# Kernel optimization log

Measured on AMD Instinct MI355X. Metric: run time of the kernel, lower is better.

## Reference

```python
import jax, jax.numpy as jnp
import numpy as np

STU, ITEM, CONC, D = 50000, 20000, 2000, 128
E_CC, E_IC, E_SI = 40000, 80000, 1000000


def _gat(tgt_x, src_x, e_src, e_dst, n_tgt, W, att_l, att_r, slope=0.2):
    # single-head GATConv, aggr='add', concat with heads=1 -> [n_tgt, D]
    if W is not None:
        xl = src_x @ W.T  # lin_l applied to source
        xr = tgt_x @ W.T  # lin_l shared for target (in_channels is int)
        # noqa: torch module uses lin_l for both when in_channels is int
    else:
        xl, xr = src_x, tgt_x
    sl = xl @ att_l  # [n_src]
    sr = xr @ att_r  # [n_tgt]
    e = sl[e_src] + sr[e_dst]
    e = jnp.where(e > 0, e, slope * e)  # leaky_relu
    # segment softmax over edges grouped by target node
    m = jax.ops.segment_max(e, e_dst, num_segments=n_tgt)
    m = jnp.where(jnp.isfinite(m), m, 0.0)
    ex = jnp.exp(e - m[e_dst])
    den = jax.ops.segment_sum(ex, e_dst, num_segments=n_tgt) + 1e-16
    alpha = ex / den[e_dst]
    return jax.ops.segment_sum(xl[e_src] * alpha[:, None], e_dst, num_segments=n_tgt)


def setup_inputs():
    key = jax.random.key(0)
    ks = jax.random.split(key, 40)
    s = 1.0 / np.sqrt(D)
    n = lambda k, sh, sc=1.0: jax.random.normal(k, sh, jnp.float32) * sc
    return {
        'stu_x': n(ks[0], (STU, D)),
        'item_x': n(ks[1], (ITEM, D)),
        'conc_x': n(ks[2], (CONC, D)),
        'stu_raw_x': n(ks[3], (STU, D)),
        'W_cc': n(ks[4], (D, D), s), 'al_cc': n(ks[5], (D,), s), 'ar_cc': n(ks[6], (D,), s),
        'W_ic': n(ks[7], (D, D), s), 'al_ic': n(ks[8], (D,), s), 'ar_ic': n(ks[9], (D,), s),
        'al_cce': n(ks[10], (D,), s), 'ar_cce': n(ks[11], (D,), s),
        'al_ice': n(ks[12], (D,), s), 'ar_ice': n(ks[13], (D,), s),
        'W_ci': n(ks[14], (D, D), s), 'al_ci': n(ks[15], (D,), s), 'ar_ci': n(ks[16], (D,), s),
        'W_si': n(ks[17], (D, D), s), 'al_si': n(ks[18], (D,), s), 'ar_si': n(ks[19], (D,), s),
        'w_ci_att': n(ks[20], (2 * D,), s), 'w_si_att': n(ks[21], (2 * D,), s),
        'W_is': n(ks[22], (D, D), s), 'al_is': n(ks[23], (D,), s), 'ar_is': n(ks[24], (D,), s),
        'cc_src': jax.random.randint(ks[25], (E_CC,), 0, CONC),
        'cc_dst': jax.random.randint(ks[26], (E_CC,), 0, CONC),
        'ic_item': jax.random.randint(ks[27], (E_IC,), 0, ITEM),
        'ic_conc': jax.random.randint(ks[28], (E_IC,), 0, CONC),
        'si_stu': jax.random.randint(ks[29], (E_SI,), 0, STU),
        'si_item': jax.random.randint(ks[30], (E_SI,), 0, ITEM),
    }


def reference(stu_x, item_x, conc_x, stu_raw_x,
              W_cc, al_cc, ar_cc, W_ic, al_ic, ar_ic,
              al_cce, ar_cce, al_ice, ar_ice,
              W_ci, al_ci, ar_ci, W_si, al_si, ar_si,
              w_ci_att, w_si_att, W_is, al_is, ar_is,
              cc_src, cc_dst, ic_item, ic_conc, si_stu, si_item):
    # --- concept fusion ---
    c1 = _gat(conc_x, conc_x, cc_src, cc_dst, CONC, W_cc, al_cc, ar_cc)   # inter_conc_conc
    c2 = _gat(conc_x, item_x, ic_item, ic_conc, CONC, W_ic, al_ic, ar_ic) # inter_item_conc
    e1 = _gat(conc_x, c1, cc_src, cc_dst, CONC, None, al_cce, ar_cce)     # exter_conc_conc (no lin)
    e2 = _gat(conc_x, c2, cc_src, cc_dst, CONC, None, al_ice, ar_ice)     # exter_item_conc (no lin)
    conc_fused = conc_x + e1 + e2
    # --- item fusion ---
    i1 = _gat(item_x, conc_x, ic_conc, ic_item, ITEM, W_ci, al_ci, ar_ci) # inter_conc_item
    i2 = _gat(item_x, stu_x, si_stu, si_item, ITEM, W_si, al_si, ar_si)   # inter_stu_item
    # softmax over dim=1 of an [N,1] tensor (as in the torch code): equals 1.0
    att1 = jax.nn.softmax((jnp.concatenate([i1, item_x], axis=1) @ w_ci_att)[:, None], axis=1)
    att2 = jax.nn.softmax((jnp.concatenate([i2, item_x], axis=1) @ w_si_att)[:, None], axis=1)
    item_fused = item_x + att1 * i1 + att2 * i2
    # --- student fusion (uses raw data['stu'].x as target) ---
    s1 = _gat(stu_raw_x, item_x, si_item, si_stu, STU, W_is, al_is, ar_is)
    stu_fused = stu_raw_x + s1
    return (conc_fused, item_fused, stu_fused)
```

## Files before the change

### kernel.cpp

```cpp
#include <hip/hip_runtime.h>

#define CONC_N 2000
#define ITEM_N 20000
#define STU_N  50000
#define NE_CC  40000
#define NE_IC  80000
#define NE_SI  1000000
#define TBUCK  382

typedef unsigned int uint;
typedef unsigned short ushort;
typedef __attribute__((ext_vector_type(8))) short bf16x8;
typedef __attribute__((ext_vector_type(4))) float f32x4;

__device__ __forceinline__ ushort f2bf(float f) {
  uint u = __float_as_uint(f);
  uint r = (u + 0x7FFFu + ((u >> 16) & 1u)) >> 16;
  return (ushort)r;
}

__device__ __forceinline__ bf16x8 packfrag(float4 lo, float4 hi) {
  union { bf16x8 s; uint u[4]; } p;
  p.u[0] = (uint)f2bf(lo.x) | ((uint)f2bf(lo.y) << 16);
  p.u[1] = (uint)f2bf(lo.z) | ((uint)f2bf(lo.w) << 16);
  p.u[2] = (uint)f2bf(hi.x) | ((uint)f2bf(hi.y) << 16);
  p.u[3] = (uint)f2bf(hi.z) | ((uint)f2bf(hi.w) << 16);
  return p.s;
}


struct CsrG {
  const int* dst; const int* src;
  unsigned* keys; int* srcs; int* offs;
  int E, n, shift, nbuck, tb, sb;
};
struct CsrGs { CsrG g[5]; };


struct ProjDesc { const float* W; const float* a; float* out; };
struct SetupArgs {
  ProjDesc p[10];
  CsrGs G;
  int* pcnt;
  const float* wsrc[5];
  ushort* wdst[5];
};

__global__ __launch_bounds__(256) void setup_k(SetupArgs A) {
  int b = blockIdx.x;
  int tid = threadIdx.x;
  if (b < 10) {
    __shared__ float Wl[128 * 132];
    __shared__ float a_s[128];
    ProjDesc d = A.p[b];
    #pragma unroll
    for (int i = 0; i < 16; ++i) {
      int s = tid + i * 256;
      int row = s >> 5, c4 = s & 31;
      float4 w = *(const float4*)&d.W[s * 4];
      float* dst = &Wl[row * 132 + c4 * 4];
      dst[0] = w.x; dst[1] = w.y; dst[2] = w.z; dst[3] = w.w;
    }
    if (tid < 128) a_s[tid] = d.a[tid];
    __syncthreads();
    if (tid < 128) {
      float acc = 0.f;
      #pragma unroll 4
      for (int j = 0; j < 128; ++j) acc += Wl[j * 132 + tid] * a_s[j];
      d.out[tid] = acc;
    }
    return;
  }
  if (b >= 170) {
    int wi = b - 170;
    const float* Ws = A.wsrc[wi];
    ushort* Wd = A.wdst[wi];
    for (int rec = tid; rec < 2048; rec += 256) {
      int lane = rec & 63;
      int kk = (rec >> 6) & 3;
      int nt = rec >> 8;
      int x = lane & 15, g = lane >> 4;
      const float* src = &Ws[(nt * 16 + x) * 128 + kk * 32 + 4 * g];
      float4 lo = *(const float4*)src;
      float4 hi = *(const float4*)(src + 16);
      bf16x8 pk = packfrag(lo, hi);
      *(bf16x8*)&Wd[rec * 8] = pk;
    }
    return;
  }
  int bsel = b - 10;
  int gi = bsel >> 5, blk = bsel & 31;
  CsrG g = A.G.g[gi];
  __shared__ int lcnt[128];
  if (tid < 128) lcnt[tid] = 0;
  __syncthreads();
  int chunk = (g.E + 31) >> 5;
  int e0 = blk * chunk, e1 = min(g.E, e0 + chunk);
  for (int e = e0 + tid; e < e1; e += 256)
    atomicAdd(&lcnt[g.dst[e] >> g.shift], 1);
  __syncthreads();
  if (tid < 128) A.pcnt[bsel * 128 + tid] = lcnt[tid];
}


__global__ __launch_bounds__(512) void csr_scan(CsrGs G, const int* __restrict__ pcnt,
                                                int* __restrict__ cur, int* __restrict__ bases) {
  __shared__ int lc[TBUCK];
  __shared__ int lb[TBUCK + 5];
  int tid = threadIdx.x, lane = tid & 63, wv = tid >> 6;
  if (tid < TBUCK) {
    int gi = 0;
    #pragma unroll
    for (int k = 1; k < 5; ++k) if (tid >= G.g[k].tb) gi = k;
    int b = tid - G.g[gi].tb;
    int s = 0;
    for (int blk = 0; blk < 32; ++blk) s += pcnt[((gi << 5) + blk) * 128 + b];
    lc[tid] = s;
  }
  __syncthreads();
  if (wv < 5) {
    CsrG g = G.g[wv];
    int carry = 0;
    for (int base = 0; base < g.nbuck; base += 64) {
      int idx = base + lane;
      int v = (idx < g.nbuck) ? lc[g.tb + idx] : 0;
      int incl = v;
      #pragma unroll
      for (int o = 1; o < 64; o <<= 1) {
        int y = __shfl_up(incl, o);
        if (lane >= o) incl += y;
      }
      if (idx < g.nbuck) lb[g.sb + idx] = carry + incl - v;
      carry += __shfl(incl, 63);
    }
    if (lane == 0) lb[g.sb + g.nbuck] = carry;
  }
  __syncthreads();
  if (tid < TBUCK + 5) bases[tid] = lb[tid];
  if (tid < TBUCK) {
    int gi = 0;
    for (int k = 1; k < 5; ++k) if (tid >= G.g[k].tb) gi = k;
    cur[tid] = lb[tid + gi];
  }
  if (tid < 5) G.g[tid].offs[G.g[tid].n] = G.g[tid].E;
}


struct GemmDesc { const float* X; ushort* Y; int n, b0; const float* dv[6]; float* dq[6]; };
struct BigC {
  GemmDesc g[5];
  int gemm_blocks;
  const float* rx; const float* rv; float* ro; int rnb;
};

__device__ void partition_body(const CsrGs& G, int* __restrict__ cur, int gi, int bx,
                               int nbx, unsigned char* smem) {
  CsrG g = G.g[gi];
  unsigned* ck = (unsigned*)smem;
  unsigned char* cb = smem + 16384;
  int* lcnt = (int*)(smem + 20480);
  int* lcur = (int*)(smem + 20992);
  int tid = threadIdx.x;
  unsigned dmask = (1u << g.shift) - 1;
  for (int c0 = bx * 4096; c0 < g.E; c0 += nbx * 4096) {
    if (tid < 128) lcnt[tid] = 0;
    __syncthreads();
    #pragma unroll
    for (int i = 0; i < 16; ++i) {
      int e = c0 + i * 256 + tid;
      if (e < g.E) {
        int d = g.dst[e], s = g.src[e];
        int b = d >> g.shift;
        ck[i * 256 + tid] = ((unsigned)(d & dmask) << 16) | (unsigned)s;
        cb[i * 256 + tid] = (unsigned char)b;
        atomicAdd(&lcnt[b], 1);
      } else cb[i * 256 + tid] = 255;
    }
    __syncthreads();
    if (tid < g.nbuck && lcnt[tid] > 0) lcur[tid] = atomicAdd(&cur[g.tb + tid], lcnt[tid]);
    __syncthreads();
    #pragma unroll
    for (int i = 0; i < 16; ++i) {
      int b = cb[i * 256 + tid];
      if (b != 255) {
        int pos = atomicAdd(&lcur[b], 1);
        g.keys[pos] = ck[i * 256 + tid];
      }
    }
    __syncthreads();
  }
}

template <int NV>
__device__ void gemm_bodyT(const GemmDesc& gd, const ushort* __restrict__ Wf, int blk) {
  int tid = threadIdx.x;
  int lane = tid & 63, wv = tid >> 6;
  int x = lane & 15, g = lane >> 4;
  int row = blk * 64 + wv * 16 + x;
  const float* xr = &gd.X[(size_t)(row < gd.n ? row : 0) * 128];
  bf16x8 afrag[4];
  float dacc[NV == 0 ? 1 : NV];
  #pragma unroll
  for (int v = 0; v < NV; ++v) dacc[v] = 0.f;
  #pragma unroll
  for (int kk = 0; kk < 4; ++kk) {
    float4 lo = *(const float4*)&xr[kk * 32 + 4 * g];
    float4 hi = *(const float4*)&xr[kk * 32 + 16 + 4 * g];
    afrag[kk] = packfrag(lo, hi);
    #pragma unroll
    for (int v = 0; v < NV; ++v) {
      const float* vp = gd.dv[v];
      float4 vlo = *(const float4*)&vp[kk * 32 + 4 * g];
      float4 vhi = *(const float4*)&vp[kk * 32 + 16 + 4 * g];
      dacc[v] += lo.x * vlo.x + lo.y * vlo.y + lo.z * vlo.z + lo.w * vlo.w
               + hi.x * vhi.x + hi.y * vhi.y + hi.z * vhi.z + hi.w * vhi.w;
    }
  }
  #pragma unroll
  for (int v = 0; v < NV; ++v) {
    float dsum = dacc[v];
    dsum += __shfl_xor(dsum, 16);
    dsum += __shfl_xor(dsum, 32);
    if (lane < 16 && row < gd.n) gd.dq[v][row] = dsum;
  }
  f32x4 acc[8];
  #pragma unroll
  for (int t = 0; t < 8; ++t) acc[t] = (f32x4){0.f, 0.f, 0.f, 0.f};
  #pragma unroll
  for (int nt = 0; nt < 8; ++nt) {
    #pragma unroll
    for (int kk = 0; kk < 4; ++kk) {
      union { uint4 u; bf16x8 s; } bu;
      bu.u = *(const uint4*)&Wf[(size_t)((nt * 4 + kk) * 64 + lane) * 8];
      acc[nt] = __builtin_amdgcn_mfma_f32_16x16x32_bf16(afrag[kk], bu.s, acc[nt], 0, 0, 0);
    }
  }
  int orow = blk * 64 + wv * 16 + 4 * g;
  #pragma unroll
  for (int r = 0; r < 4; ++r) {
    int gr = orow + r;
    if (gr < gd.n) {
      #pragma unroll
      for (int nt = 0; nt < 8; ++nt)
        gd.Y[(size_t)gr * 128 + nt * 16 + x] = f2bf(acc[nt][r]);
    }
  }
}

__device__ void rdot_body(const float* __restrict__ x, const float* __restrict__ v,
                          float* __restrict__ o, int n, int blk, int nblk) {
  int lane = threadIdx.x & 63;
  int wid = (blk * 256 + threadIdx.x) >> 6;
  int nw = nblk * 4;
  float va = v[lane], vb = v[64 + lane];
  for (int r = wid; r < n; r += nw) {
    float a = x[r * 128 + lane] * va + x[r * 128 + 64 + lane] * vb;
    #pragma unroll
    for (int of = 32; of; of >>= 1) a += __shfl_xor(a, of);
    if (lane == 0) o[r] = a;
  }
}

__global__ __launch_bounds__(256, 2) void mid2_k(CsrGs G, int* cur, BigC C,
                                                 const ushort* W0, const ushort* W1,
                                                 const ushort* W2, const ushort* W3,
                                                 const ushort* W4) {
  __shared__ __align__(16) unsigned char smem[21504];
  int b = blockIdx.x;
  if (b < 600) {
    partition_body(G, cur, b / 120, b % 120, 120, smem);
    return;
  }
  b -= 600;
  if (b < C.gemm_blocks) {
    if (b < C.g[1].b0)      gemm_bodyT<6>(C.g[0], W0, b - C.g[0].b0);
    else if (b < C.g[2].b0) gemm_bodyT<4>(C.g[1], W1, b - C.g[1].b0);
    else if (b < C.g[3].b0) gemm_bodyT<0>(C.g[2], W2, b - C.g[2].b0);
    else if (b < C.g[4].b0) gemm_bodyT<1>(C.g[3], W3, b - C.g[3].b0);
    else                    gemm_bodyT<0>(C.g[4], W4, b - C.g[4].b0);
  } else {
    rdot_body(C.rx, C.rv, C.ro, STU_N, b - C.gemm_blocks, C.rnb);
  }
}


__global__ __launch_bounds__(256) void csr_build(CsrGs G, const int* __restrict__ bases) {
  int bid = blockIdx.x;
  int gi = 0;
  for (int k = 1; k < 5; ++k) if (bid >= G.g[k].tb) gi = k;
  CsrG g = G.g[gi];
  int b = bid - g.tb;
  int base = bases[g.sb + b];
  int cnt = bases[g.sb + b + 1] - base;
  if (cnt > 16384) cnt = 16384;

  __shared__ unsigned lkeys[16384];
  __shared__ int lh[512], lex[512], lcu[512], wsum[4];
  int tid = threadIdx.x;
  lh[tid] = 0; lh[tid + 256] = 0;
  __syncthreads();
  for (int j = tid; j < cnt; j += 256) {
    unsigned k = g.keys[base + j];
    lkeys[j] = k;
    atomicAdd(&lh[k >> 16], 1);
  }
  __syncthreads();
  int a0 = lh[2 * tid], a1 = lh[2 * tid + 1];
  int pair = a0 + a1;
  int lane = tid & 63, wv = tid >> 6;
  int incl = pair;
  #pragma unroll
  for (int o = 1; o < 64; o <<= 1) {
    int y = __shfl_up(incl, o);
    if (lane >= o) incl += y;
  }
  if (lane == 63) wsum[wv] = incl;
  __syncthreads();
  if (tid == 0) {
    int s = 0;
    #pragma unroll
    for (int w = 0; w < 4; ++w) { int t = wsum[w]; wsum[w] = s; s += t; }
  }
  __syncthreads();
  int ep = wsum[wv] + incl - pair;
  lex[2 * tid] = ep;       lex[2 * tid + 1] = ep + a0;
  lcu[2 * tid] = ep;       lcu[2 * tid + 1] = ep + a0;
  __syncthreads();
  int dst0 = b << g.shift;
  int ndst = min(1 << g.shift, g.n - dst0);
  for (int dl = tid; dl < ndst; dl += 256) g.offs[dst0 + dl] = base + lex[dl];
  for (int j = tid; j < cnt; j += 256) {
    unsigned k = lkeys[j];
    int dl = k >> 16;
    int pos = atomicAdd(&lcu[dl], 1);
    g.srcs[base + pos] = (int)(k & 0xFFFFu);
  }
}


__device__ __forceinline__ void fma8(float acc[8], float wj, uint4 u) {
  acc[0] += wj * __uint_as_float(u.x << 16);
  acc[1] += wj * __uint_as_float(u.x & 0xFFFF0000u);
  acc[2] += wj * __uint_as_float(u.y << 16);
  acc[3] += wj * __uint_as_float(u.y & 0xFFFF0000u);
  acc[4] += wj * __uint_as_float(u.z << 16);
  acc[5] += wj * __uint_as_float(u.z & 0xFFFF0000u);
  acc[6] += wj * __uint_as_float(u.w << 16);
  acc[7] += wj * __uint_as_float(u.w & 0xFFFF0000u);
}

__device__ void gat_core_bf(const int* __restrict__ offs, const int* __restrict__ srcs,
                            const float* __restrict__ sl, const float* __restrict__ sr,
                            const uint* __restrict__ xl, int t, int lane, float acc[8]) {
  int sbeg = offs[t], send = offs[t + 1];
  float srt = sr[t];
  int i0l = sbeg + lane;
  bool act0 = i0l < send;
  int s0 = act0 ? srcs[i0l] : 0;
  float e0;
  {
    float e = sl[s0] + srt;
    e = e > 0.f ? e : 0.2f * e;
    e0 = act0 ? e : -1e30f;
  }
  float m = e0, se = act0 ? 1.f : 0.f;
  for (int i = i0l + 64; i < send; i += 64) {
    int s = srcs[i];
    float e = sl[s] + srt;
    e = e > 0.f ? e : 0.2f * e;
    float mn = fmaxf(m, e);
    se = se * __expf(m - mn) + __expf(e - mn);
    m = mn;
  }
  #pragma unroll
  for (int o = 32; o; o >>= 1) {
    float m2 = __shfl_xor(m, o), s2 = __shfl_xor(se, o);
    float mn = fmaxf(m, m2);
    se = se * __expf(m - mn) + s2 * __expf(m2 - mn);
    m = mn;
  }
  float inv = 1.f / (se + 1e-16f);

  int g = lane & 15;
  int q = lane >> 4;
  #pragma unroll
  for (int r = 0; r < 8; ++r) acc[r] = 0.f;

  for (int i0 = sbeg; i0 < send; i0 += 64) {
    int cnt = min(64, send - i0);
    int s; float wgt;
    if (i0 == sbeg) {
      s = s0;
      wgt = act0 ? __expf(e0 - m) * inv : 0.f;
    } else {
      s = 0; wgt = 0.f;
      if (lane < cnt) {
        s = srcs[i0 + lane];
        float e = sl[s] + srt;
        e = e > 0.f ? e : 0.2f * e;
        wgt = __expf(e - m) * inv;
      }
    }
    int kmax = (cnt + 3) >> 2;
    int k = 0;
    for (; k + 4 <= kmax; k += 4) {
      int e0i = 4 * k + q;
      int sj0 = __shfl(s, e0i);
      int sj1 = __shfl(s, e0i + 4);
      int sj2 = __shfl(s, e0i + 8);
      int sj3 = __shfl(s, e0i + 12);
      float wj0 = __shfl(wgt, e0i);
      float wj1 = __shfl(wgt, e0i + 4);
      float wj2 = __shfl(wgt, e0i + 8);
      float wj3 = __shfl(wgt, e0i + 12);
      uint4 u0 = *(const uint4*)&xl[(size_t)sj0 * 64 + g * 4];
      uint4 u1 = *(const uint4*)&xl[(size_t)sj1 * 64 + g * 4];
      uint4 u2 = *(const uint4*)&xl[(size_t)sj2 * 64 + g * 4];
      uint4 u3 = *(const uint4*)&xl[(size_t)sj3 * 64 + g * 4];
      fma8(acc, wj0, u0);
      fma8(acc, wj1, u1);
      fma8(acc, wj2, u2);
      fma8(acc, wj3, u3);
    }
    for (; k < kmax; ++k) {
      int ej = 4 * k + q;
      int sj = __shfl(s, ej);
      float wj = __shfl(wgt, ej);
      uint4 u = *(const uint4*)&xl[(size_t)sj * 64 + g * 4];
      fma8(acc, wj, u);
    }
  }
  #pragma unroll
  for (int r = 0; r < 8; ++r) {
    acc[r] += __shfl_xor(acc[r], 16);
    acc[r] += __shfl_xor(acc[r], 32);
  }
}

__device__ __forceinline__ void gat_store(const float acc[8], const float* base0,
                                          float* out, int t, int lane) {
  int g = lane & 15;
  if (lane < 16) {
    int d = t * 128 + g * 8;
    float4 a0 = make_float4(acc[0], acc[1], acc[2], acc[3]);
    float4 a1 = make_float4(acc[4], acc[5], acc[6], acc[7]);
    if (base0) {
      const float4 b0 = *(const float4*)&base0[d];
      const float4 b1 = *(const float4*)&base0[d + 4];
      a0.x += b0.x; a0.y += b0.y; a0.z += b0.z; a0.w += b0.w;
      a1.x += b1.x; a1.y += b1.y; a1.z += b1.z; a1.w += b1.w;
    }
    *(float4*)&out[d] = a0;
    *(float4*)&out[d + 4] = a1;
  }
}

__device__ void c1c2_body(const int* offs, const int* srcs, const float* sl,
                          const float* sr, const uint* xl, const float* al,
                          float* o, float* slo, int t, int lane) {
  float acc[8];
  gat_core_bf(offs, srcs, sl, sr, xl, t, lane, acc);
  int g = lane & 15;
  float4 v0 = *(const float4*)&al[g * 8];
  float4 v1 = *(const float4*)&al[g * 8 + 4];
  float p = acc[0] * v0.x + acc[1] * v0.y + acc[2] * v0.z + acc[3] * v0.w +
            acc[4] * v1.x + acc[5] * v1.y + acc[6] * v1.z + acc[7] * v1.w;
  #pragma unroll
  for (int o2 = 8; o2; o2 >>= 1) p += __shfl_xor(p, o2);
  if (lane == 0) slo[t] = p;
  if (lane < 16) {
    int d = t * 128 + g * 8;
    *(float4*)&o[d] = make_float4(acc[0], acc[1], acc[2], acc[3]);
    *(float4*)&o[d + 4] = make_float4(acc[4], acc[5], acc[6], acc[7]);
  }
}

__device__ void gat_dual_core(const int* __restrict__ offs, const int* __restrict__ srcs,
                              const float* __restrict__ sl1, const float* __restrict__ sr1,
                              const float* __restrict__ xl1,
                              const float* __restrict__ sl2, const float* __restrict__ sr2,
                              const float* __restrict__ xl2,
                              const float* __restrict__ base,
                              float* __restrict__ out, int t, int lane) {
  int sbeg = offs[t], send = offs[t + 1];
  float srt1 = sr1[t], srt2 = sr2[t];
  float m1 = -1e30f, m2 = -1e30f;
  for (int i = sbeg + lane; i < send; i += 64) {
    int s = srcs[i];
    float e1 = sl1[s] + srt1; e1 = e1 > 0.f ? e1 : 0.2f * e1;
    float e2 = sl2[s] + srt2; e2 = e2 > 0.f ? e2 : 0.2f * e2;
    m1 = fmaxf(m1, e1); m2 = fmaxf(m2, e2);
  }
  #pragma unroll
  for (int o = 32; o; o >>= 1) {
    m1 = fmaxf(m1, __shfl_xor(m1, o));
    m2 = fmaxf(m2, __shfl_xor(m2, o));
  }
  float se1 = 0.f, se2 = 0.f;
  for (int i = sbeg + lane; i < send; i += 64) {
    int s = srcs[i];
    float e1 = sl1[s] + srt1; e1 = e1 > 0.f ? e1 : 0.2f * e1;
    float e2 = sl2[s] + srt2; e2 = e2 > 0.f ? e2 : 0.2f * e2;
    se1 += __expf(e1 - m1); se2 += __expf(e2 - m2);
  }
  #pragma unroll
  for (int o = 32; o; o >>= 1) {
    se1 += __shfl_xor(se1, o);
    se2 += __shfl_xor(se2, o);
  }
  float inv1 = 1.f / (se1 + 1e-16f), inv2 = 1.f / (se2 + 1e-16f);
  float ax = 0.f, ay = 0.f;
  for (int i0 = sbeg; i0 < send; i0 += 64) {
    int cnt = min(64, send - i0);
    int s = 0; float w1 = 0.f, w2 = 0.f;
    if (lane < cnt) {
      s = srcs[i0 + lane];
      float e1 = sl1[s] + srt1; e1 = e1 > 0.f ? e1 : 0.2f * e1;
      float e2 = sl2[s] + srt2; e2 = e2 > 0.f ? e2 : 0.2f * e2;
      w1 = __expf(e1 - m1) * inv1;
      w2 = __expf(e2 - m2) * inv2;
    }
    for (int j = 0; j < cnt; ++j) {
      int sj = __shfl(s, j);
      float wj1 = __shfl(w1, j);
      float wj2 = __shfl(w2, j);
      const float2 v1 = *(const float2*)&xl1[sj * 128 + lane * 2];
      const float2 v2 = *(const float2*)&xl2[sj * 128 + lane * 2];
      ax += wj1 * v1.x + wj2 * v2.x;
      ay += wj1 * v1.y + wj2 * v2.y;
    }
  }
  const float2 b = *(const float2*)&base[t * 128 + lane * 2];
  float2 o2; o2.x = ax + b.x; o2.y = ay + b.y;
  *(float2*)&out[t * 128 + lane * 2] = o2;
}


#define NB_S1  12500
#define NB_I12 5000

struct GatsArgs {
  const int *offs4, *srcs4; const float *sl_is, *sr_is; const uint* xl_is;
  const float* stu_raw_x; float* out_stu;
  const int *offs3, *srcs3; const float *sl_si, *sr_si; const uint* xl_si;
  const int *offs2, *srcs2; const float *sl_ci, *sr_ci; const uint* xl_ci;
  const float* item_x; float* out_item;
  const int *offs0, *srcs0; const float *sl_cc, *sr_cc; const uint* xl_cc;
  const float* al_cce; float *c1, *sl_cce;
  const int *offs1, *srcs1; const float *sl_ic, *sr_ic; const uint* xl_ic;
  const float* al_ice; float *c2, *sl_ice;
};

__global__ void gats_k(GatsArgs A) {
  int b = blockIdx.x;
  int lane = threadIdx.x & 63;
  if (b < NB_S1) {
    int t = (b * blockDim.x + threadIdx.x) >> 6;
    if (t >= STU_N) return;
    float acc[8];
    gat_core_bf(A.offs4, A.srcs4, A.sl_is, A.sr_is, A.xl_is, t, lane, acc);
    gat_store(acc, A.stu_raw_x, A.out_stu, t, lane);
  } else if (b < NB_S1 + NB_I12) {
    int t = ((b - NB_S1) * blockDim.x + threadIdx.x) >> 6;
    if (t >= ITEM_N) return;
    float acc1[8], acc2[8];
    gat_core_bf(A.offs2, A.srcs2, A.sl_ci, A.sr_ci, A.xl_ci, t, lane, acc1);
    gat_core_bf(A.offs3, A.srcs3, A.sl_si, A.sr_si, A.xl_si, t, lane, acc2);
    #pragma unroll
    for (int r = 0; r < 8; ++r) acc1[r] += acc2[r];
    gat_store(acc1, A.item_x, A.out_item, t, lane);
  } else {
    int sub = b - NB_S1 - NB_I12;
    int which = sub >= 500;
    int t = ((sub - which * 500) * blockDim.x + threadIdx.x) >> 6;
    if (t >= CONC_N) return;
    if (!which)
      c1c2_body(A.offs0, A.srcs0, A.sl_cc, A.sr_cc, A.xl_cc, A.al_cce, A.c1, A.sl_cce, t, lane);
    else
      c1c2_body(A.offs1, A.srcs1, A.sl_ic, A.sr_ic, A.xl_ic, A.al_ice, A.c2, A.sl_ice, t, lane);
  }
}


__global__ void fin_k(const int* offs0, const int* srcs0,
                      const float* sl_cce, const float* sr_cce, const float* c1,
                      const float* sl_ice, const float* sr_ice, const float* c2,
                      const float* conc_x, float* out_conc) {
  int t = (blockIdx.x * blockDim.x + threadIdx.x) >> 6;
  if (t >= CONC_N) return;
  gat_dual_core(offs0, srcs0, sl_cce, sr_cce, c1, sl_ice, sr_ice, c2,
                conc_x, out_conc, t, threadIdx.x & 63);
}


extern "C" void kernel_launch(void* const* d_in, const int* in_sizes, int n_in,
                              void* d_out, int out_size, void* d_ws, size_t ws_size,
                              hipStream_t stream) {
  const float* stu_x     = (const float*)d_in[0];
  const float* item_x    = (const float*)d_in[1];
  const float* conc_x    = (const float*)d_in[2];
  const float* stu_raw_x = (const float*)d_in[3];
  const float* W_cc  = (const float*)d_in[4];
  const float* al_cc = (const float*)d_in[5];
  const float* ar_cc = (const float*)d_in[6];
  const float* W_ic  = (const float*)d_in[7];
  const float* al_ic = (const float*)d_in[8];
  const float* ar_ic = (const float*)d_in[9];
  const float* al_cce = (const float*)d_in[10];
  const float* ar_cce = (const float*)d_in[11];
  const float* al_ice = (const float*)d_in[12];
  const float* ar_ice = (const float*)d_in[13];
  const float* W_ci  = (const float*)d_in[14];
  const float* al_ci = (const float*)d_in[15];
  const float* ar_ci = (const float*)d_in[16];
  const float* W_si  = (const float*)d_in[17];
  const float* al_si = (const float*)d_in[18];
  const float* ar_si = (const float*)d_in[19];
  const float* W_is  = (const float*)d_in[22];
  const float* al_is = (const float*)d_in[23];
  const float* ar_is = (const float*)d_in[24];
  const int* cc_src  = (const int*)d_in[25];
  const int* cc_dst  = (const int*)d_in[26];
  const int* ic_item = (const int*)d_in[27];
  const int* ic_conc = (const int*)d_in[28];
  const int* si_stu  = (const int*)d_in[29];
  const int* si_item = (const int*)d_in[30];

  char* wsb = (char*)d_ws;
  size_t off = 0;
  auto alloc = [&](size_t bytes) -> void* {
    void* p = wsb + off;
    off = (off + bytes + 255) & ~(size_t)255;
    return p;
  };

  ushort* concWcc = (ushort*)alloc((size_t)CONC_N * 128 * 2);
  ushort* itemWic = (ushort*)alloc((size_t)ITEM_N * 128 * 2);
  ushort* concWci = (ushort*)alloc((size_t)CONC_N * 128 * 2);
  ushort* stuWsi  = (ushort*)alloc((size_t)STU_N  * 128 * 2);
  ushort* itemWis = (ushort*)alloc((size_t)ITEM_N * 128 * 2);
  ushort* Wbf[5];
  for (int i = 0; i < 5; ++i) Wbf[i] = (ushort*)alloc(128 * 128 * 2);
  float* c1buf   = (float*)alloc((size_t)CONC_N * 128 * 4);
  float* c2buf   = (float*)alloc((size_t)CONC_N * 128 * 4);
  float* vecs    = (float*)alloc(10 * 128 * 4);
  float* sl_cc  = (float*)alloc(CONC_N * 4);
  float* sr_cc  = (float*)alloc(CONC_N * 4);
  float* sl_ic  = (float*)alloc(ITEM_N * 4);
  float* sr_ic  = (float*)alloc(CONC_N * 4);
  float* sl_ci  = (float*)alloc(CONC_N * 4);
  float* sr_ci  = (float*)alloc(ITEM_N * 4);
  float* sl_si  = (float*)alloc(STU_N * 4);
  float* sr_si  = (float*)alloc(ITEM_N * 4);
  float* sl_is  = (float*)alloc(ITEM_N * 4);
  float* sr_is  = (float*)alloc(STU_N * 4);
  float* sl_cce = (float*)alloc(CONC_N * 4);
  float* sr_cce = (float*)alloc(CONC_N * 4);
  float* sl_ice = (float*)alloc(CONC_N * 4);
  float* sr_ice = (float*)alloc(CONC_N * 4);

  unsigned* keys0 = (unsigned*)alloc((size_t)NE_CC * 4);
  unsigned* keys1 = (unsigned*)alloc((size_t)NE_IC * 4);
  unsigned* keys2 = (unsigned*)alloc((size_t)NE_IC * 4);
  unsigned* keys3 = (unsigned*)alloc((size_t)NE_SI * 4);
  unsigned* keys4 = (unsigned*)alloc((size_t)NE_SI * 4);
  int* srcs0 = (int*)alloc((size_t)NE_CC * 4);
  int* srcs1 = (int*)alloc((size_t)NE_IC * 4);
  int* srcs2 = (int*)alloc((size_t)NE_IC * 4);
  int* srcs3 = (int*)alloc((size_t)NE_SI * 4);
  int* srcs4 = (int*)alloc((size_t)NE_SI * 4);
  int* offs0 = (int*)alloc((CONC_N + 1) * 4);
  int* offs1 = (int*)alloc((CONC_N + 1) * 4);
  int* offs2 = (int*)alloc((ITEM_N + 1) * 4);
  int* offs3 = (int*)alloc((ITEM_N + 1) * 4);
  int* offs4 = (int*)alloc((STU_N + 1) * 4);
  int* pcnt      = (int*)alloc(5 * 32 * 128 * 4);
  int* cur_all   = (int*)alloc(TBUCK * 4);
  int* bases_all = (int*)alloc((TBUCK + 5) * 4);

  float* out = (float*)d_out;
  float* out_conc = out;
  float* out_item = out + (size_t)CONC_N * 128;
  float* out_stu  = out + (size_t)(CONC_N + ITEM_N) * 128;

  CsrGs G;
  G.g[0] = {cc_dst,  cc_src,  keys0, srcs0, offs0, NE_CC, CONC_N, 5, 63,   0,   0};
  G.g[1] = {ic_conc, ic_item, keys1, srcs1, offs1, NE_IC, CONC_N, 5, 63,  63,  64};
  G.g[2] = {ic_item, ic_conc, keys2, srcs2, offs2, NE_IC, ITEM_N, 8, 79, 126, 128};
  G.g[3] = {si_item, si_stu,  keys3, srcs3, offs3, NE_SI, ITEM_N, 8, 79, 205, 208};
  G.g[4] = {si_stu,  si_item, keys4, srcs4, offs4, NE_SI, STU_N,  9, 98, 284, 288};

  SetupArgs SA;
  SA.p[0] = {W_cc, al_cc, vecs + 0 * 128};
  SA.p[1] = {W_cc, ar_cc, vecs + 1 * 128};
  SA.p[2] = {W_ic, al_ic, vecs + 2 * 128};
  SA.p[3] = {W_ic, ar_ic, vecs + 3 * 128};
  SA.p[4] = {W_ci, al_ci, vecs + 4 * 128};
  SA.p[5] = {W_ci, ar_ci, vecs + 5 * 128};
  SA.p[6] = {W_si, al_si, vecs + 6 * 128};
  SA.p[7] = {W_si, ar_si, vecs + 7 * 128};
  SA.p[8] = {W_is, al_is, vecs + 8 * 128};
  SA.p[9] = {W_is, ar_is, vecs + 9 * 128};
  SA.G = G;
  SA.pcnt = pcnt;
  SA.wsrc[0] = W_cc; SA.wsrc[1] = W_ic; SA.wsrc[2] = W_ci;
  SA.wsrc[3] = W_si; SA.wsrc[4] = W_is;
  for (int i = 0; i < 5; ++i) SA.wdst[i] = Wbf[i];
  setup_k<<<175, 256, 0, stream>>>(SA);

  csr_scan<<<1, 512, 0, stream>>>(G, pcnt, cur_all, bases_all);

  BigC C;
  C.g[0] = {conc_x, concWcc, CONC_N, 0,
            {vecs + 0 * 128, vecs + 1 * 128, vecs + 3 * 128, vecs + 4 * 128, ar_cce, ar_ice},
            {sl_cc, sr_cc, sr_ic, sl_ci, sr_cce, sr_ice}};
  C.g[1] = {item_x, itemWic, ITEM_N, 32,
            {vecs + 2 * 128, vecs + 5 * 128, vecs + 7 * 128, vecs + 8 * 128, nullptr, nullptr},
            {sl_ic, sr_ci, sr_si, sl_is, nullptr, nullptr}};
  C.g[2] = {conc_x, concWci, CONC_N, 345,
            {nullptr, nullptr, nullptr, nullptr, nullptr, nullptr},
            {nullptr, nullptr, nullptr, nullptr, nullptr, nullptr}};
  C.g[3] = {stu_x, stuWsi, STU_N, 377,
            {vecs + 6 * 128, nullptr, nullptr, nullptr, nullptr, nullptr},
            {sl_si, nullptr, nullptr, nullptr, nullptr, nullptr}};
  C.g[4] = {item_x, itemWis, ITEM_N, 1159,
            {nullptr, nullptr, nullptr, nullptr, nullptr, nullptr},
            {nullptr, nullptr, nullptr, nullptr, nullptr, nullptr}};
  C.gemm_blocks = 1472;
  C.rx = stu_raw_x; C.rv = vecs + 9 * 128; C.ro = sr_is; C.rnb = 1024;
  mid2_k<<<600 + 2496, 256, 0, stream>>>(G, cur_all, C, Wbf[0], Wbf[1], Wbf[2], Wbf[3], Wbf[4]);

  csr_build<<<TBUCK, 256, 0, stream>>>(G, bases_all);

  GatsArgs GA;
  GA.offs4 = offs4; GA.srcs4 = srcs4; GA.sl_is = sl_is; GA.sr_is = sr_is;
  GA.xl_is = (const uint*)itemWis; GA.stu_raw_x = stu_raw_x; GA.out_stu = out_stu;
  GA.offs3 = offs3; GA.srcs3 = srcs3; GA.sl_si = sl_si; GA.sr_si = sr_si;
  GA.xl_si = (const uint*)stuWsi;
  GA.offs2 = offs2; GA.srcs2 = srcs2; GA.sl_ci = sl_ci; GA.sr_ci = sr_ci;
  GA.xl_ci = (const uint*)concWci; GA.item_x = item_x; GA.out_item = out_item;
  GA.offs0 = offs0; GA.srcs0 = srcs0; GA.sl_cc = sl_cc; GA.sr_cc = sr_cc;
  GA.xl_cc = (const uint*)concWcc; GA.al_cce = al_cce; GA.c1 = c1buf; GA.sl_cce = sl_cce;
  GA.offs1 = offs1; GA.srcs1 = srcs1; GA.sl_ic = sl_ic; GA.sr_ic = sr_ic;
  GA.xl_ic = (const uint*)itemWic; GA.al_ice = al_ice; GA.c2 = c2buf; GA.sl_ice = sl_ice;
  gats_k<<<NB_S1 + NB_I12 + 1000, 256, 0, stream>>>(GA);

  fin_k<<<500, 256, 0, stream>>>(offs0, srcs0, sl_cce, sr_cce, c1buf,
                                 sl_ice, sr_ice, c2buf, conc_x, out_conc);
}
```

Before: 208.8 us.

## Process four target nodes per wavefront with 16-lane groups in GAT aggregation

New measurement: 207.0 us. No clear change (-0.8%).

```diff
diff --git a/kernel.cpp b/kernel.cpp
--- a/kernel.cpp
+++ b/kernel.cpp
@@ -349,12 +349,18 @@
   acc[7] += wj * __uint_as_float(u.w & 0xFFFF0000u);
 }
 
-__device__ void gat_core_bf(const int* __restrict__ offs, const int* __restrict__ srcs,
-                            const float* __restrict__ sl, const float* __restrict__ sr,
-                            const uint* __restrict__ xl, int t, int lane, float acc[8]) {
-  int sbeg = offs[t], send = offs[t + 1];
-  float srt = sr[t];
-  int i0l = sbeg + lane;
+__device__ void gat_core16(const int* __restrict__ offs, const int* __restrict__ srcs,
+                           const float* __restrict__ sl, const float* __restrict__ sr,
+                           const uint* __restrict__ xl, int t4, int n_tgt, int lane,
+                           float acc[8]) {
+  int q = lane >> 4, il = lane & 15;
+  int t = t4 + q;
+  bool tv = t < n_tgt;
+  int sbeg = tv ? offs[t] : 0;
+  int send = tv ? offs[t + 1] : 0;
+  float srt = tv ? sr[t] : 0.f;
+
+  int i0l = sbeg + il;
   bool act0 = i0l < send;
   int s0 = act0 ? srcs[i0l] : 0;
   float e0;
@@ -364,7 +370,7 @@
     e0 = act0 ? e : -1e30f;
   }
   float m = e0, se = act0 ? 1.f : 0.f;
-  for (int i = i0l + 64; i < send; i += 64) {
+  for (int i = i0l + 16; i < send; i += 16) {
     int s = srcs[i];
     float e = sl[s] + srt;
     e = e > 0.f ? e : 0.2f * e;
@@ -373,7 +379,7 @@
     m = mn;
   }
   #pragma unroll
-  for (int o = 32; o; o >>= 1) {
+  for (int o = 8; o; o >>= 1) {
     float m2 = __shfl_xor(m, o), s2 = __shfl_xor(se, o);
     float mn = fmaxf(m, m2);
     se = se * __expf(m - mn) + s2 * __expf(m2 - mn);
@@ -381,95 +387,69 @@
   }
   float inv = 1.f / (se + 1e-16f);
 
-  int g = lane & 15;
-  int q = lane >> 4;
   #pragma unroll
   for (int r = 0; r < 8; ++r) acc[r] = 0.f;
 
-  for (int i0 = sbeg; i0 < send; i0 += 64) {
-    int cnt = min(64, send - i0);
+  int qb = q << 4;
+  for (int i0 = sbeg; i0 < send; i0 += 16) {
+    int cnt = min(16, send - i0);
     int s; float wgt;
     if (i0 == sbeg) {
       s = s0;
       wgt = act0 ? __expf(e0 - m) * inv : 0.f;
     } else {
       s = 0; wgt = 0.f;
-      if (lane < cnt) {
-        s = srcs[i0 + lane];
+      if (il < cnt) {
+        s = srcs[i0 + il];
         float e = sl[s] + srt;
         e = e > 0.f ? e : 0.2f * e;
         wgt = __expf(e - m) * inv;
       }
     }
-    int kmax = (cnt + 3) >> 2;
-    int k = 0;
-    for (; k + 4 <= kmax; k += 4) {
-      int e0i = 4 * k + q;
-      int sj0 = __shfl(s, e0i);
-      int sj1 = __shfl(s, e0i + 4);
-      int sj2 = __shfl(s, e0i + 8);
-      int sj3 = __shfl(s, e0i + 12);
-      float wj0 = __shfl(wgt, e0i);
-      float wj1 = __shfl(wgt, e0i + 4);
-      float wj2 = __shfl(wgt, e0i + 8);
-      float wj3 = __shfl(wgt, e0i + 12);
-      uint4 u0 = *(const uint4*)&xl[(size_t)sj0 * 64 + g * 4];
-      uint4 u1 = *(const uint4*)&xl[(size_t)sj1 * 64 + g * 4];
-      uint4 u2 = *(const uint4*)&xl[(size_t)sj2 * 64 + g * 4];
-      uint4 u3 = *(const uint4*)&xl[(size_t)sj3 * 64 + g * 4];
-      fma8(acc, wj0, u0);
-      fma8(acc, wj1, u1);
-      fma8(acc, wj2, u2);
-      fma8(acc, wj3, u3);
-    }
-    for (; k < kmax; ++k) {
-      int ej = 4 * k + q;
-      int sj = __shfl(s, ej);
-      float wj = __shfl(wgt, ej);
-      uint4 u = *(const uint4*)&xl[(size_t)sj * 64 + g * 4];
+    #pragma unroll 2
+    for (int j = 0; j < cnt; ++j) {
+      int sj = __shfl(s, qb + j);
+      float wj = __shfl(wgt, qb + j);
+      uint4 u = *(const uint4*)&xl[(size_t)sj * 64 + il * 4];
       fma8(acc, wj, u);
     }
   }
-  #pragma unroll
-  for (int r = 0; r < 8; ++r) {
-    acc[r] += __shfl_xor(acc[r], 16);
-    acc[r] += __shfl_xor(acc[r], 32);
-  }
-}
-
-__device__ __forceinline__ void gat_store(const float acc[8], const float* base0,
-                                          float* out, int t, int lane) {
-  int g = lane & 15;
-  if (lane < 16) {
-    int d = t * 128 + g * 8;
-    float4 a0 = make_float4(acc[0], acc[1], acc[2], acc[3]);
-    float4 a1 = make_float4(acc[4], acc[5], acc[6], acc[7]);
-    if (base0) {
-      const float4 b0 = *(const float4*)&base0[d];
-      const float4 b1 = *(const float4*)&base0[d + 4];
-      a0.x += b0.x; a0.y += b0.y; a0.z += b0.z; a0.w += b0.w;
-      a1.x += b1.x; a1.y += b1.y; a1.z += b1.z; a1.w += b1.w;
-    }
-    *(float4*)&out[d] = a0;
-    *(float4*)&out[d + 4] = a1;
-  }
-}
-
-__device__ void c1c2_body(const int* offs, const int* srcs, const float* sl,
-                          const float* sr, const uint* xl, const float* al,
-                          float* o, float* slo, int t, int lane) {
+}
+
+__device__ __forceinline__ void gat_store16(const float acc[8], const float* base0,
+                                            float* out, int t4, int n_tgt, int lane) {
+  int q = lane >> 4, il = lane & 15;
+  int t = t4 + q;
+  if (t >= n_tgt) return;
+  int d = t * 128 + il * 8;
+  float4 a0 = make_float4(acc[0], acc[1], acc[2], acc[3]);
+  float4 a1 = make_float4(acc[4], acc[5], acc[6], acc[7]);
+  if (base0) {
+    const float4 b0 = *(const float4*)&base0[d];
+    const float4 b1 = *(const float4*)&base0[d + 4];
+    a0.x += b0.x; a0.y += b0.y; a0.z += b0.z; a0.w += b0.w;
+    a1.x += b1.x; a1.y += b1.y; a1.z += b1.z; a1.w += b1.w;
+  }
+  *(float4*)&out[d] = a0;
+  *(float4*)&out[d + 4] = a1;
+}
+
+__device__ void c1c2_body16(const int* offs, const int* srcs, const float* sl,
+                            const float* sr, const uint* xl, const float* al,
+                            float* o, float* slo, int t4, int n_tgt, int lane) {
   float acc[8];
-  gat_core_bf(offs, srcs, sl, sr, xl, t, lane, acc);
-  int g = lane & 15;
-  float4 v0 = *(const float4*)&al[g * 8];
-  float4 v1 = *(const float4*)&al[g * 8 + 4];
+  gat_core16(offs, srcs, sl, sr, xl, t4, n_tgt, lane, acc);
+  int q = lane >> 4, il = lane & 15;
+  int t = t4 + q;
+  float4 v0 = *(const float4*)&al[il * 8];
+  float4 v1 = *(const float4*)&al[il * 8 + 4];
   float p = acc[0] * v0.x + acc[1] * v0.y + acc[2] * v0.z + acc[3] * v0.w +
             acc[4] * v1.x + acc[5] * v1.y + acc[6] * v1.z + acc[7] * v1.w;
   #pragma unroll
   for (int o2 = 8; o2; o2 >>= 1) p += __shfl_xor(p, o2);
-  if (lane == 0) slo[t] = p;
-  if (lane < 16) {
-    int d = t * 128 + g * 8;
+  if (t < n_tgt) {
+    if (il == 0) slo[t] = p;
+    int d = t * 128 + il * 8;
     *(float4*)&o[d] = make_float4(acc[0], acc[1], acc[2], acc[3]);
     *(float4*)&o[d + 4] = make_float4(acc[4], acc[5], acc[6], acc[7]);
   }
@@ -536,8 +516,9 @@
 }
 
 
-#define NB_S1  12500
-#define NB_I12 5000
+#define NB_S1  3125
+#define NB_I12 1250
+#define NB_CC  125
 
 struct GatsArgs {
   const int *offs4, *srcs4; const float *sl_is, *sr_is; const uint* xl_is;
@@ -554,30 +535,30 @@
 __global__ void gats_k(GatsArgs A) {
   int b = blockIdx.x;
   int lane = threadIdx.x & 63;
+  int wv = threadIdx.x >> 6;
   if (b < NB_S1) {
-    int t = (b * blockDim.x + threadIdx.x) >> 6;
-    if (t >= STU_N) return;
+    int t4 = b * 16 + wv * 4;
     float acc[8];
-    gat_core_bf(A.offs4, A.srcs4, A.sl_is, A.sr_is, A.xl_is, t, lane, acc);
-    gat_store(acc, A.stu_raw_x, A.out_stu, t, lane);
+    gat_core16(A.offs4, A.srcs4, A.sl_is, A.sr_is, A.xl_is, t4, STU_N, lane, acc);
+    gat_store16(acc, A.stu_raw_x, A.out_stu, t4, STU_N, lane);
   } else if (b < NB_S1 + NB_I12) {
-    int t = ((b - NB_S1) * blockDim.x + threadIdx.x) >> 6;
-    if (t >= ITEM_N) return;
+    int t4 = (b - NB_S1) * 16 + wv * 4;
     float acc1[8], acc2[8];
-    gat_core_bf(A.offs2, A.srcs2, A.sl_ci, A.sr_ci, A.xl_ci, t, lane, acc1);
-    gat_core_bf(A.offs3, A.srcs3, A.sl_si, A.sr_si, A.xl_si, t, lane, acc2);
+    gat_core16(A.offs2, A.srcs2, A.sl_ci, A.sr_ci, A.xl_ci, t4, ITEM_N, lane, acc1);
+    gat_core16(A.offs3, A.srcs3, A.sl_si, A.sr_si, A.xl_si, t4, ITEM_N, lane, acc2);
     #pragma unroll
     for (int r = 0; r < 8; ++r) acc1[r] += acc2[r];
-    gat_store(acc1, A.item_x, A.out_item, t, lane);
+    gat_store16(acc1, A.item_x, A.out_item, t4, ITEM_N, lane);
   } else {
     int sub = b - NB_S1 - NB_I12;
-    int which = sub >= 500;
-    int t = ((sub - which * 500) * blockDim.x + threadIdx.x) >> 6;
-    if (t >= CONC_N) return;
+    int which = sub >= NB_CC;
+    int t4 = (sub - which * NB_CC) * 16 + wv * 4;
     if (!which)
-      c1c2_body(A.offs0, A.srcs0, A.sl_cc, A.sr_cc, A.xl_cc, A.al_cce, A.c1, A.sl_cce, t, lane);
+      c1c2_body16(A.offs0, A.srcs0, A.sl_cc, A.sr_cc, A.xl_cc, A.al_cce,
+                  A.c1, A.sl_cce, t4, CONC_N, lane);
     else
-      c1c2_body(A.offs1, A.srcs1, A.sl_ic, A.sr_ic, A.xl_ic, A.al_ice, A.c2, A.sl_ice, t, lane);
+      c1c2_body16(A.offs1, A.srcs1, A.sl_ic, A.sr_ic, A.xl_ic, A.al_ice,
+                  A.c2, A.sl_ice, t4, CONC_N, lane);
   }
 }
 
@@ -743,7 +724,7 @@
   GA.xl_cc = (const uint*)concWcc; GA.al_cce = al_cce; GA.c1 = c1buf; GA.sl_cce = sl_cce;
   GA.offs1 = offs1; GA.srcs1 = srcs1; GA.sl_ic = sl_ic; GA.sr_ic = sr_ic;
   GA.xl_ic = (const uint*)itemWic; GA.al_ice = al_ice; GA.c2 = c2buf; GA.sl_ice = sl_ice;
-  gats_k<<<NB_S1 + NB_I12 + 1000, 256, 0, stream>>>(GA);
+  gats_k<<<NB_S1 + NB_I12 + 2 * NB_CC, 256, 0, stream>>>(GA);
 
   fin_k<<<500, 256, 0, stream>>>(offs0, srcs0, sl_cce, sr_cce, c1buf,
                                  sl_ice, sr_ice, c2buf, conc_x, out_conc);
```
